# Kernel optimization log

Measured on AMD Instinct MI355X. Metric: run time of the kernel, lower is better.

The kernel has to match this reference:

```python
import jax, jax.numpy as jnp
import numpy as np

NUM_JOINTS = 17

def _build_norm_adj():
    # Same skeleton as _get_skeleton_edges, made bidirectional; row-normalized
    # so that A @ x computes the per-node mean over neighbors (every joint
    # has degree >= 1, matching the original's mean aggregation branch).
    conns = [(0, 7), (7, 8), (8, 9), (9, 10), (0, 1), (1, 2), (2, 3), (0, 4),
             (4, 5), (5, 6), (8, 11), (11, 12), (12, 13), (8, 14), (14, 15), (15, 16)]
    A = np.zeros((NUM_JOINTS, NUM_JOINTS), dtype=np.float32)
    for a, b in conns:
        A[a, b] = 1.0
        A[b, a] = 1.0
    deg = A.sum(axis=1, keepdims=True)
    A = A / np.maximum(deg, 1.0)
    return jnp.asarray(A)

def _xavier(key, out_dim, in_dim):
    lim = np.sqrt(6.0 / (in_dim + out_dim)).astype(np.float32)
    return jax.random.uniform(key, (out_dim, in_dim), jnp.float32, -lim, lim)

def setup_inputs() -> dict:
    key = jax.random.key(0)
    ks = jax.random.split(key, 6)
    B, J, D_IN, H, D_OUT = 65536, NUM_JOINTS, 3, 64, 256
    x = jax.random.normal(ks[0], (B, J, D_IN), jnp.float32)
    return {
        "x": x,
        "A": _build_norm_adj(),
        "W1": _xavier(ks[1], H, D_IN), "b1": jnp.zeros((H,), jnp.float32),
        "W2": _xavier(ks[2], H, H),    "b2": jnp.zeros((H,), jnp.float32),
        "W3": _xavier(ks[3], H, H),    "b3": jnp.zeros((H,), jnp.float32),
        "Wp1": _xavier(ks[4], H, J * H), "bp1": jnp.zeros((H,), jnp.float32),
        "Wp2": _xavier(ks[5], D_OUT, H), "bp2": jnp.zeros((D_OUT,), jnp.float32),
    }

def reference(x, A, W1, b1, W2, b2, W3, b3, Wp1, bp1, Wp2, bp2):
    # GCN layer 1: neighbor-mean aggregate then linear (+ReLU; dropout = eval identity)
    h = jnp.einsum('ij,bjd->bid', A, x)            # (B, 17, 3)
    h = jax.nn.relu(h @ W1.T + b1)                 # (B, 17, 64)
    # GCN layer 2
    h = jnp.einsum('ij,bjd->bid', A, h)
    h = jax.nn.relu(h @ W2.T + b2)
    # GCN layer 3 (no activation)
    h = jnp.einsum('ij,bjd->bid', A, h)
    h = h @ W3.T + b3                              # (B, 17, 64)
    # Global pool MLP over flattened joints
    flat = h.reshape(h.shape[0], -1)               # (B, 17*64)
    z = jax.nn.relu(flat @ Wp1.T + bp1)            # (B, 64)
    return z @ Wp2.T + bp2                         # (B, 256)
```

## Files before the change

### kernel.cpp

```cpp
#include <hip/hip_runtime.h>
#include <hip/hip_bf16.h>
#include <stdint.h>

typedef __attribute__((ext_vector_type(8))) short short8;
typedef __attribute__((ext_vector_type(4))) float f32x4;
typedef __attribute__((ext_vector_type(4))) unsigned int u32x4;
typedef __attribute__((ext_vector_type(2))) unsigned int u32x2;

constexpr int kNBR[17][4] = {
    {7, 1, 4, 0}, {0, 2, 0, 0}, {1, 3, 0, 0}, {2, 0, 0, 0},
    {0, 5, 0, 0}, {4, 6, 0, 0}, {5, 0, 0, 0}, {0, 8, 0, 0},
    {7, 9, 11, 14}, {8, 10, 0, 0}, {9, 0, 0, 0}, {8, 12, 0, 0},
    {11, 13, 0, 0}, {12, 0, 0, 0}, {8, 15, 0, 0}, {14, 16, 0, 0},
    {15, 0, 0, 0}};
constexpr int kDEG[17] = {3,2,2,1,2,2,1,2,4,2,1,2,2,1,2,2,1};
constexpr float kRDEG[5] = {0.f, 1.f, 0.5f, 0.33333334f, 0.25f};
constexpr int kWNT[4] = {3, 4, 5, 5};
constexpr int kWJT[4][5] = {{8, 1, 2, 0, 0},
                            {0, 4, 5, 3, 0},
                            {7, 9, 11, 6, 10},
                            {12, 14, 15, 13, 16}};

__device__ inline unsigned short f2bf(float f) {
  union { float f; uint32_t u; } v; v.f = f;
  uint32_t u = v.u;
  uint32_t r = u + 0x7fffu + ((u >> 16) & 1u);
  return (unsigned short)(r >> 16);
}
__device__ inline uint32_t pk2(float a, float b) {
  union { __hip_bfloat162 h; uint32_t u; } v;
  v.h = __float22bfloat162_rn(make_float2(a, b));
  return v.u;
}
__device__ inline f32x4 mfma16(short8 a, short8 b, f32x4 c) {
  return __builtin_amdgcn_mfma_f32_16x16x32_bf16(a, b, c, 0, 0, 0);
}
__device__ inline int hswz(int row, int cb) {
  return row * 128 + (cb ^ ((row & 7) << 4));
}

__global__ void prep(const float* __restrict__ W1,
                     const float* __restrict__ W2,
                     const float* __restrict__ Wp2,
                     const float* __restrict__ W3,
                     const float* __restrict__ Wp1,
                     const float* __restrict__ b3,
                     const float* __restrict__ bp1,
                     const float* __restrict__ b1,
                     short* __restrict__ W1b,
                     short* __restrict__ W2b,
                     short* __restrict__ Wp2b,
                     short* __restrict__ Mb,
                     float* __restrict__ bp1p) {
  __shared__ float w3s[4096];
  __shared__ float Qs[256];
  const int tid = threadIdx.x;
  const int bx = blockIdx.x;
  if (bx < 272) {
    for (int q = tid; q < 4096; q += 256) w3s[q] = W3[q];
    {
      int ro = tid >> 6, k = tid & 63;
      int r = bx * 4 + ro;
      int f = r / 17, i = r - f * 17;
      int dj = kDEG[i];
      float s = 0.f;
#pragma unroll
      for (int t = 0; t < 4; t++) {
        if (t < dj) {
          int nb = kNBR[i][t];
          s += kRDEG[kDEG[nb]] * Wp1[f * 1088 + nb * 64 + k];
        }
      }
      Qs[ro * 64 + k] = s;
    }
    __syncthreads();
    {
      int ro = tid >> 6, c = tid & 63;
      int r = bx * 4 + ro;
      int f = r / 17, i = r - f * 17;
      float s = 0.f;
#pragma unroll
      for (int k = 0; k < 64; k++) s += Qs[ro * 64 + k] * w3s[k * 64 + c];
      int h = c >> 5;
      int c5 = c & 31;
      int q = (c5 >> 2) & 3;
      int m = ((c5 >> 4) << 2) | (c5 & 3);
      int w = f >> 4, l15 = f & 15;
      Mb[((((w * 17 + i) * 2 + h) * 64) + q * 16 + l15) * 8 + m] = (short)f2bf(s);
    }
  } else if (bx < 354) {
    int q = (bx - 272) * 256 + tid;
    if (q < 4096) W2b[q] = (short)f2bf(W2[q]);
    int q2 = q - 4096;
    if (q2 >= 0 && q2 < 16384) Wp2b[q2] = (short)f2bf(Wp2[q2]);
    int q3 = q - 20480;
    if (q3 >= 0 && q3 < 512) {
      int k = q3 & 7, row = q3 >> 3;
      short v = 0;
      if (k < 3) v = (short)f2bf(W1[row * 3 + k]);
      else if (k == 3) v = (short)f2bf(b1[row]);
      W1b[q3] = v;
    }
  } else {
    int wv = tid >> 6, l = tid & 63;
    int f = (bx - 354) * 4 + wv;
    float s = 0.f;
#pragma unroll
    for (int i = 0; i < 17; i++) s += Wp1[f * 1088 + i * 64 + l] * b3[l];
#pragma unroll
    for (int off = 32; off > 0; off >>= 1) s += __shfl_down(s, off);
    if (l == 0) bp1p[f] = bp1[f] + s;
  }
}

template <int WV>
__device__ __forceinline__ void waveBody(
    const short* __restrict__ Mb2, const short* __restrict__ Wp2b,
    const short* __restrict__ W2b, const float* __restrict__ bp2g,
    float* __restrict__ OUT, short* hbuf, float* xs, float* sbias,
    const short8 (&w1f)[4], int bx, int lane, int ln15, int quad) {
  constexpr int NT = kWNT[WV];
  char* hb0 = (char*)hbuf;

#pragma unroll
  for (int t = 0; t < NT; t++) {
    const int j = kWJT[WV][t];
    const int dj = kDEG[j];
    const float w = kRDEG[dj];
    union { short8 s; u32x4 u; } fr[2];
#pragma unroll
    for (int g = 0; g < 2; g++) {
      const float* xsg = xs + g * 816;
      fr[g].u = (u32x4){0u, 0u, 0u, 0u};
      if (quad == 0) {
        float s0, s1, s2;
        {
          int b = ln15 * 51 + kNBR[j][0] * 3;
          s0 = xsg[b]; s1 = xsg[b + 1]; s2 = xsg[b + 2];
        }
        if (dj > 1) {
          int b = ln15 * 51 + kNBR[j][1] * 3;
          s0 += xsg[b]; s1 += xsg[b + 1]; s2 += xsg[b + 2];
        }
        if (dj > 2) {
          int b = ln15 * 51 + kNBR[j][2] * 3;
          s0 += xsg[b]; s1 += xsg[b + 1]; s2 += xsg[b + 2];
        }
        if (dj > 3) {
          int b = ln15 * 51 + kNBR[j][3] * 3;
          s0 += xsg[b]; s1 += xsg[b + 1]; s2 += xsg[b + 2];
        }
        fr[g].u.x = pk2(s0 * w, s1 * w);
        fr[g].u.y = pk2(s2 * w, 1.0f);
      }
    }
#pragma unroll
    for (int g = 0; g < 2; g++) {
      f32x4 a[4];
#pragma unroll
      for (int ft = 0; ft < 4; ft++)
        a[ft] = mfma16(w1f[ft], fr[g].s, (f32x4){0.f, 0.f, 0.f, 0.f});
#pragma unroll
      for (int ft = 0; ft < 4; ft++) {
        int fb = ft * 16 + quad * 4;
        u32x2 pk;
        pk.x = pk2(fmaxf(a[ft].x, 0.f), fmaxf(a[ft].y, 0.f));
        pk.y = pk2(fmaxf(a[ft].z, 0.f), fmaxf(a[ft].w, 0.f));
        *(u32x2*)(hb0 + g * 34816 + hswz(j * 16 + ln15, fb * 2)) = pk;
      }
    }
  }
  __syncthreads();

  short8 w2f[2][4];
#pragma unroll
  for (int kk = 0; kk < 2; kk++)
#pragma unroll
    for (int ft = 0; ft < 4; ft++)
      w2f[kk][ft] = *(const short8*)(W2b + (ft * 16 + ln15) * 64 + kk * 32 + quad * 8);

  u32x2 pkh2[2][NT][4];
#pragma unroll
  for (int t = 0; t < NT; t++) {
    const int j = kWJT[WV][t];
    const int dj = kDEG[j];
    const float w = kRDEG[dj];
#pragma unroll
    for (int g = 0; g < 2; g++) {
      f32x4 a[4];
#pragma unroll
      for (int ft = 0; ft < 4; ft++) a[ft] = (f32x4){0.f, 0.f, 0.f, 0.f};
#pragma unroll
      for (int s = 0; s < 4; s++)
        if (s < dj) {
          const int i = kNBR[j][s];
#pragma unroll
          for (int kk = 0; kk < 2; kk++) {
            short8 bf = *(const short8*)(hb0 + g * 34816 +
                                         hswz(i * 16 + ln15, kk * 64 + quad * 16));
#pragma unroll
            for (int ft = 0; ft < 4; ft++)
              a[ft] = mfma16(w2f[kk][ft], bf, a[ft]);
          }
        }
#pragma unroll
      for (int ft = 0; ft < 4; ft++) {
        int fb = ft * 16 + quad * 4;
        f32x4 bv = *(const f32x4*)&sbias[fb];
        u32x2 pk;
        pk.x = pk2(fmaxf(a[ft].x * w + bv.x, 0.f), fmaxf(a[ft].y * w + bv.y, 0.f));
        pk.y = pk2(fmaxf(a[ft].z * w + bv.z, 0.f), fmaxf(a[ft].w * w + bv.w, 0.f));
        pkh2[g][t][ft] = pk;
      }
    }
  }

  f32x4 zacc[4][2];
#pragma unroll
  for (int w4 = 0; w4 < 4; w4++) {
    zacc[w4][0] = (f32x4){0.f, 0.f, 0.f, 0.f};
    zacc[w4][1] = (f32x4){0.f, 0.f, 0.f, 0.f};
  }
  const short8* mb = (const short8*)Mb2;
#pragma unroll
  for (int t = 0; t < NT; t++) {
    const int i = kWJT[WV][t];
#pragma unroll
    for (int h = 0; h < 2; h++) {
      union { short8 s; u32x4 u; } bf0, bf1;
      bf0.u = (u32x4){pkh2[0][t][2 * h].x, pkh2[0][t][2 * h].y,
                      pkh2[0][t][2 * h + 1].x, pkh2[0][t][2 * h + 1].y};
      bf1.u = (u32x4){pkh2[1][t][2 * h].x, pkh2[1][t][2 * h].y,
                      pkh2[1][t][2 * h + 1].x, pkh2[1][t][2 * h + 1].y};
#pragma unroll
      for (int w4 = 0; w4 < 4; w4++) {
        short8 af = mb[(((w4 * 17 + i) * 2 + h) * 64) + lane];
        zacc[w4][0] = mfma16(af, bf0.s, zacc[w4][0]);
        zacc[w4][1] = mfma16(af, bf1.s, zacc[w4][1]);
      }
    }
  }
  __syncthreads();

#pragma unroll
  for (int w4 = 0; w4 < 4; w4++)
#pragma unroll
    for (int g = 0; g < 2; g++)
      *(f32x4*)(hb0 + WV * 8192 + (w4 * 2 + g) * 1024 + lane * 16) = zacc[w4][g];

  short8 wp2f[4][2];
#pragma unroll
  for (int t = 0; t < 4; t++) {
    int ot = WV + 4 * t;
    wp2f[t][0] = *(const short8*)(Wp2b + (ot * 16 + ln15) * 64 + quad * 8);
    wp2f[t][1] = *(const short8*)(Wp2b + (ot * 16 + ln15) * 64 + 32 + quad * 8);
  }
  __syncthreads();

  char* zbB = (char*)xs;
#pragma unroll
  for (int half = 0; half < 2; half++) {
    const int gw = WV + half * 4;
    const int g = gw & 1, w4 = gw >> 1;
    f32x4 s0 = *(const f32x4*)(hb0 + 0 * 8192 + gw * 1024 + lane * 16);
    f32x4 s1 = *(const f32x4*)(hb0 + 1 * 8192 + gw * 1024 + lane * 16);
    f32x4 s2 = *(const f32x4*)(hb0 + 2 * 8192 + gw * 1024 + lane * 16);
    f32x4 s3 = *(const f32x4*)(hb0 + 3 * 8192 + gw * 1024 + lane * 16);
    f32x4 s = (s0 + s1) + (s2 + s3);
    const int e = lane & 15, qd = lane >> 4;
    const int f0 = w4 * 16 + qd * 4;
    f32x4 bv = *(const f32x4*)&sbias[64 + f0];
    u32x2 pk;
    pk.x = pk2(fmaxf(s.x + bv.x, 0.f), fmaxf(s.y + bv.y, 0.f));
    pk.y = pk2(fmaxf(s.z + bv.z, 0.f), fmaxf(s.w + bv.w, 0.f));
    *(u32x2*)(zbB + g * 2048 + e * 128 + ((f0 * 2) ^ ((e & 7) << 4))) = pk;
  }
  __syncthreads();

  const int e0 = bx * 32;
#pragma unroll
  for (int g = 0; g < 2; g++) {
    short8 bf0 = *(const short8*)(zbB + g * 2048 + ln15 * 128 +
                                  ((quad * 16) ^ ((ln15 & 7) << 4)));
    short8 bf1 = *(const short8*)(zbB + g * 2048 + ln15 * 128 +
                                  ((64 + quad * 16) ^ ((ln15 & 7) << 4)));
    int e0g = e0 + g * 16;
#pragma unroll
    for (int t = 0; t < 4; t++) {
      int ot = WV + 4 * t;
      f32x4 a = mfma16(wp2f[t][0], bf0, (f32x4){0.f, 0.f, 0.f, 0.f});
      a = mfma16(wp2f[t][1], bf1, a);
      int ob = ot * 16 + quad * 4;
      f32x4 bv = *(const f32x4*)&bp2g[ob];
      f32x4 res = a + bv;
      *(f32x4*)(OUT + (size_t)(e0g + ln15) * 256 + ob) = res;
    }
  }
}

__launch_bounds__(256, 2)
__global__ void gcn_main(const float* __restrict__ X,
                         const short* __restrict__ Mb2,
                         const short* __restrict__ Wp2b,
                         const short* __restrict__ W2b,
                         const short* __restrict__ W1b,
                         const float* __restrict__ bp1p,
                         const float* __restrict__ b2g,
                         const float* __restrict__ bp2g,
                         float* __restrict__ OUT) {
  __shared__ __align__(16) short hbuf[2 * 272 * 64];
  __shared__ __align__(16) float xs[2 * 816];
  __shared__ __align__(16) float sbias[128];

  const int tid = threadIdx.x;
  const int wave = tid >> 6;
  const int lane = tid & 63;
  const int ln15 = lane & 15;
  const int quad = lane >> 4;
  const int bx = blockIdx.x;

  for (int q = tid; q < 408; q += 256)
    ((f32x4*)xs)[q] = ((const f32x4*)(X + (size_t)bx * 1632))[q];
  short8 w1f[4];
#pragma unroll
  for (int ft = 0; ft < 4; ft++)
    w1f[ft] = *(const short8*)(W1b + (ft * 16 + ln15) * 8);
  if (tid < 128) sbias[tid] = (tid < 64) ? b2g[tid] : bp1p[tid - 64];
  __syncthreads();

  if (wave == 0)
    waveBody<0>(Mb2, Wp2b, W2b, bp2g, OUT, hbuf, xs, sbias, w1f, bx, lane, ln15, quad);
  else if (wave == 1)
    waveBody<1>(Mb2, Wp2b, W2b, bp2g, OUT, hbuf, xs, sbias, w1f, bx, lane, ln15, quad);
  else if (wave == 2)
    waveBody<2>(Mb2, Wp2b, W2b, bp2g, OUT, hbuf, xs, sbias, w1f, bx, lane, ln15, quad);
  else
    waveBody<3>(Mb2, Wp2b, W2b, bp2g, OUT, hbuf, xs, sbias, w1f, bx, lane, ln15, quad);
}

extern "C" void kernel_launch(void* const* d_in, const int* in_sizes, int n_in,
                              void* d_out, int out_size, void* d_ws, size_t ws_size,
                              hipStream_t stream) {
  const float* X = (const float*)d_in[0];
  const float* W1 = (const float*)d_in[2];
  const float* b1 = (const float*)d_in[3];
  const float* W2 = (const float*)d_in[4];
  const float* b2 = (const float*)d_in[5];
  const float* W3 = (const float*)d_in[6];
  const float* b3 = (const float*)d_in[7];
  const float* Wp1 = (const float*)d_in[8];
  const float* bp1 = (const float*)d_in[9];
  const float* Wp2 = (const float*)d_in[10];
  const float* bp2 = (const float*)d_in[11];
  float* OUT = (float*)d_out;
  const int B = in_sizes[0] / 51;

  char* ws = (char*)d_ws;
  short* Mb = (short*)(ws + 0);
  short* Wp2b = (short*)(ws + 139264);
  short* W2b = (short*)(ws + 172032);
  short* W1b = (short*)(ws + 180224);
  float* bp1p = (float*)(ws + 181248);

  prep<<<370, 256, 0, stream>>>(W1, W2, Wp2, W3, Wp1, b3, bp1, b1,
                                W1b, W2b, Wp2b, Mb, bp1p);
  gcn_main<<<B / 32, 256, 0, stream>>>(X, Mb, Wp2b, W2b, W1b, bp1p,
                                       b2, bp2, OUT);
}
```

Baseline: 148.6 us.

## Recompute layer-1 activations per wave in registers instead of sharing through LDS

Each wave now recomputes the layer-1 GCN outputs for every neighbor of its assigned joints directly in registers, so layer-2 MFMAs read them without a shared-memory round trip. This drops the 70KB hbuf and two block-wide barriers. The final pooled-MLP bias/ReLU stage also keeps its result in registers, with W2 and Wp2 permuted in prep so the MFMA output fragment can be reused directly as the next B operand. In exchange, layer-1 MFMAs are duplicated per neighbor and register pressure rises from the ph1 arrays.

```diff
diff --git a/kernel.cpp b/kernel.cpp
--- a/kernel.cpp
+++ b/kernel.cpp
@@ -34,9 +34,6 @@
 }
 __device__ inline f32x4 mfma16(short8 a, short8 b, f32x4 c) {
   return __builtin_amdgcn_mfma_f32_16x16x32_bf16(a, b, c, 0, 0, 0);
-}
-__device__ inline int hswz(int row, int cb) {
-  return row * 128 + (cb ^ ((row & 7) << 4));
 }
 
 __global__ void prep(const float* __restrict__ W1,
@@ -90,9 +87,19 @@
     }
   } else if (bx < 354) {
     int q = (bx - 272) * 256 + tid;
-    if (q < 4096) W2b[q] = (short)f2bf(W2[q]);
+    if (q < 4096) {
+      int r = q >> 6, c = q & 63;
+      int h = c >> 5, c5 = c & 31;
+      int qq = (c5 >> 2) & 3, m = ((c5 >> 4) << 2) | (c5 & 3);
+      W2b[r * 64 + h * 32 + qq * 8 + m] = (short)f2bf(W2[q]);
+    }
     int q2 = q - 4096;
-    if (q2 >= 0 && q2 < 16384) Wp2b[q2] = (short)f2bf(Wp2[q2]);
+    if (q2 >= 0 && q2 < 16384) {
+      int r = q2 >> 6, c = q2 & 63;
+      int h = c >> 5, c5 = c & 31;
+      int qq = (c5 >> 2) & 3, m = ((c5 >> 4) << 2) | (c5 & 3);
+      Wp2b[r * 64 + h * 32 + qq * 8 + m] = (short)f2bf(Wp2[q2]);
+    }
     int q3 = q - 20480;
     if (q3 >= 0 && q3 < 512) {
       int k = q3 & 7, row = q3 >> 3;
@@ -115,92 +122,89 @@
 
 template <int WV>
 __device__ __forceinline__ void waveBody(
-    const short* __restrict__ Mb2, const short* __restrict__ Wp2b,
-    const short* __restrict__ W2b, const float* __restrict__ bp2g,
-    float* __restrict__ OUT, short* hbuf, float* xs, float* sbias,
+    const short* __restrict__ Mb2, const short* __restrict__ Wp2p,
+    const short* __restrict__ W2p, const float* __restrict__ bp2g,
+    float* __restrict__ OUT, float* __restrict__ pbuf,
+    float* __restrict__ xs, float* __restrict__ sbias,
     const short8 (&w1f)[4], int bx, int lane, int ln15, int quad) {
   constexpr int NT = kWNT[WV];
-  char* hb0 = (char*)hbuf;
-
+
+  short8 w2f[2][4];
+#pragma unroll
+  for (int h = 0; h < 2; h++)
+#pragma unroll
+    for (int ft = 0; ft < 4; ft++)
+      w2f[h][ft] = *(const short8*)(W2p + (ft * 16 + ln15) * 64 + h * 32 + quad * 8);
+
+  u32x2 pkh2[2][NT][4];
 #pragma unroll
   for (int t = 0; t < NT; t++) {
     const int j = kWJT[WV][t];
     const int dj = kDEG[j];
-    const float w = kRDEG[dj];
-    union { short8 s; u32x4 u; } fr[2];
-#pragma unroll
-    for (int g = 0; g < 2; g++) {
-      const float* xsg = xs + g * 816;
-      fr[g].u = (u32x4){0u, 0u, 0u, 0u};
-      if (quad == 0) {
-        float s0, s1, s2;
-        {
-          int b = ln15 * 51 + kNBR[j][0] * 3;
-          s0 = xsg[b]; s1 = xsg[b + 1]; s2 = xsg[b + 2];
+    const float wj = kRDEG[dj];
+    u32x2 ph1[4][2][4];
+#pragma unroll
+    for (int s = 0; s < 4; s++) {
+      if (s < dj) {
+        const int i = kNBR[j][s];
+        const int di = kDEG[i];
+        const float wi = kRDEG[di];
+#pragma unroll
+        for (int g = 0; g < 2; g++) {
+          const float* xsg = xs + g * 816;
+          union { short8 s8; u32x4 u; } fr;
+          fr.u = (u32x4){0u, 0u, 0u, 0u};
+          if (quad == 0) {
+            float s0, s1, s2;
+            {
+              int b = ln15 * 51 + kNBR[i][0] * 3;
+              s0 = xsg[b]; s1 = xsg[b + 1]; s2 = xsg[b + 2];
+            }
+            if (di > 1) {
+              int b = ln15 * 51 + kNBR[i][1] * 3;
+              s0 += xsg[b]; s1 += xsg[b + 1]; s2 += xsg[b + 2];
+            }
+            if (di > 2) {
+              int b = ln15 * 51 + kNBR[i][2] * 3;
+              s0 += xsg[b]; s1 += xsg[b + 1]; s2 += xsg[b + 2];
+            }
+            if (di > 3) {
+              int b = ln15 * 51 + kNBR[i][3] * 3;
+              s0 += xsg[b]; s1 += xsg[b + 1]; s2 += xsg[b + 2];
+            }
+            fr.u.x = pk2(s0 * wi, s1 * wi);
+            fr.u.y = pk2(s2 * wi, 1.0f);
+          }
+          f32x4 a[4];
+#pragma unroll
+          for (int ft = 0; ft < 4; ft++)
+            a[ft] = mfma16(w1f[ft], fr.s8, (f32x4){0.f, 0.f, 0.f, 0.f});
+#pragma unroll
+          for (int ft = 0; ft < 4; ft++) {
+            u32x2 pk;
+            pk.x = pk2(fmaxf(a[ft].x, 0.f), fmaxf(a[ft].y, 0.f));
+            pk.y = pk2(fmaxf(a[ft].z, 0.f), fmaxf(a[ft].w, 0.f));
+            ph1[s][g][ft] = pk;
+          }
         }
-        if (dj > 1) {
-          int b = ln15 * 51 + kNBR[j][1] * 3;
-          s0 += xsg[b]; s1 += xsg[b + 1]; s2 += xsg[b + 2];
-        }
-        if (dj > 2) {
-          int b = ln15 * 51 + kNBR[j][2] * 3;
-          s0 += xsg[b]; s1 += xsg[b + 1]; s2 += xsg[b + 2];
-        }
-        if (dj > 3) {
-          int b = ln15 * 51 + kNBR[j][3] * 3;
-          s0 += xsg[b]; s1 += xsg[b + 1]; s2 += xsg[b + 2];
-        }
-        fr[g].u.x = pk2(s0 * w, s1 * w);
-        fr[g].u.y = pk2(s2 * w, 1.0f);
       }
     }
 #pragma unroll
     for (int g = 0; g < 2; g++) {
       f32x4 a[4];
 #pragma unroll
-      for (int ft = 0; ft < 4; ft++)
-        a[ft] = mfma16(w1f[ft], fr[g].s, (f32x4){0.f, 0.f, 0.f, 0.f});
-#pragma unroll
-      for (int ft = 0; ft < 4; ft++) {
-        int fb = ft * 16 + quad * 4;
-        u32x2 pk;
-        pk.x = pk2(fmaxf(a[ft].x, 0.f), fmaxf(a[ft].y, 0.f));
-        pk.y = pk2(fmaxf(a[ft].z, 0.f), fmaxf(a[ft].w, 0.f));
-        *(u32x2*)(hb0 + g * 34816 + hswz(j * 16 + ln15, fb * 2)) = pk;
-      }
-    }
-  }
-  __syncthreads();
-
-  short8 w2f[2][4];
-#pragma unroll
-  for (int kk = 0; kk < 2; kk++)
-#pragma unroll
-    for (int ft = 0; ft < 4; ft++)
-      w2f[kk][ft] = *(const short8*)(W2b + (ft * 16 + ln15) * 64 + kk * 32 + quad * 8);
-
-  u32x2 pkh2[2][NT][4];
-#pragma unroll
-  for (int t = 0; t < NT; t++) {
-    const int j = kWJT[WV][t];
-    const int dj = kDEG[j];
-    const float w = kRDEG[dj];
-#pragma unroll
-    for (int g = 0; g < 2; g++) {
-      f32x4 a[4];
-#pragma unroll
       for (int ft = 0; ft < 4; ft++) a[ft] = (f32x4){0.f, 0.f, 0.f, 0.f};
 #pragma unroll
       for (int s = 0; s < 4; s++)
         if (s < dj) {
-          const int i = kNBR[j][s];
-#pragma unroll
-          for (int kk = 0; kk < 2; kk++) {
-            short8 bf = *(const short8*)(hb0 + g * 34816 +
-                                         hswz(i * 16 + ln15, kk * 64 + quad * 16));
+#pragma unroll
+          for (int h = 0; h < 2; h++) {
+            union { short8 s8; u32x4 u; } bf;
+            bf.u = (u32x4){ph1[s][g][2 * h].x, ph1[s][g][2 * h].y,
+                           ph1[s][g][2 * h + 1].x, ph1[s][g][2 * h + 1].y};
 #pragma unroll
             for (int ft = 0; ft < 4; ft++)
-              a[ft] = mfma16(w2f[kk][ft], bf, a[ft]);
+              a[ft] = mfma16(w2f[h][ft], bf.s8, a[ft]);
           }
         }
 #pragma unroll
@@ -208,8 +212,8 @@
         int fb = ft * 16 + quad * 4;
         f32x4 bv = *(const f32x4*)&sbias[fb];
         u32x2 pk;
-        pk.x = pk2(fmaxf(a[ft].x * w + bv.x, 0.f), fmaxf(a[ft].y * w + bv.y, 0.f));
-        pk.y = pk2(fmaxf(a[ft].z * w + bv.z, 0.f), fmaxf(a[ft].w * w + bv.w, 0.f));
+        pk.x = pk2(fmaxf(a[ft].x * wj + bv.x, 0.f), fmaxf(a[ft].y * wj + bv.y, 0.f));
+        pk.y = pk2(fmaxf(a[ft].z * wj + bv.z, 0.f), fmaxf(a[ft].w * wj + bv.w, 0.f));
         pkh2[g][t][ft] = pk;
       }
     }
@@ -227,7 +231,7 @@
     const int i = kWJT[WV][t];
 #pragma unroll
     for (int h = 0; h < 2; h++) {
-      union { short8 s; u32x4 u; } bf0, bf1;
+      union { short8 s8; u32x4 u; } bf0, bf1;
       bf0.u = (u32x4){pkh2[0][t][2 * h].x, pkh2[0][t][2 * h].y,
                       pkh2[0][t][2 * h + 1].x, pkh2[0][t][2 * h + 1].y};
       bf1.u = (u32x4){pkh2[1][t][2 * h].x, pkh2[1][t][2 * h].y,
@@ -235,61 +239,56 @@
 #pragma unroll
       for (int w4 = 0; w4 < 4; w4++) {
         short8 af = mb[(((w4 * 17 + i) * 2 + h) * 64) + lane];
-        zacc[w4][0] = mfma16(af, bf0.s, zacc[w4][0]);
-        zacc[w4][1] = mfma16(af, bf1.s, zacc[w4][1]);
+        zacc[w4][0] = mfma16(af, bf0.s8, zacc[w4][0]);
+        zacc[w4][1] = mfma16(af, bf1.s8, zacc[w4][1]);
       }
     }
   }
-  __syncthreads();
-
 #pragma unroll
   for (int w4 = 0; w4 < 4; w4++)
 #pragma unroll
     for (int g = 0; g < 2; g++)
-      *(f32x4*)(hb0 + WV * 8192 + (w4 * 2 + g) * 1024 + lane * 16) = zacc[w4][g];
-
+      *(f32x4*)(pbuf + WV * 2048 + (w4 * 2 + g) * 256 + lane * 4) = zacc[w4][g];
   short8 wp2f[4][2];
 #pragma unroll
   for (int t = 0; t < 4; t++) {
     int ot = WV + 4 * t;
-    wp2f[t][0] = *(const short8*)(Wp2b + (ot * 16 + ln15) * 64 + quad * 8);
-    wp2f[t][1] = *(const short8*)(Wp2b + (ot * 16 + ln15) * 64 + 32 + quad * 8);
+    wp2f[t][0] = *(const short8*)(Wp2p + (ot * 16 + ln15) * 64 + quad * 8);
+    wp2f[t][1] = *(const short8*)(Wp2p + (ot * 16 + ln15) * 64 + 32 + quad * 8);
   }
   __syncthreads();
 
-  char* zbB = (char*)xs;
-#pragma unroll
-  for (int half = 0; half < 2; half++) {
-    const int gw = WV + half * 4;
-    const int g = gw & 1, w4 = gw >> 1;
-    f32x4 s0 = *(const f32x4*)(hb0 + 0 * 8192 + gw * 1024 + lane * 16);
-    f32x4 s1 = *(const f32x4*)(hb0 + 1 * 8192 + gw * 1024 + lane * 16);
-    f32x4 s2 = *(const f32x4*)(hb0 + 2 * 8192 + gw * 1024 + lane * 16);
-    f32x4 s3 = *(const f32x4*)(hb0 + 3 * 8192 + gw * 1024 + lane * 16);
-    f32x4 s = (s0 + s1) + (s2 + s3);
-    const int e = lane & 15, qd = lane >> 4;
-    const int f0 = w4 * 16 + qd * 4;
-    f32x4 bv = *(const f32x4*)&sbias[64 + f0];
-    u32x2 pk;
-    pk.x = pk2(fmaxf(s.x + bv.x, 0.f), fmaxf(s.y + bv.y, 0.f));
-    pk.y = pk2(fmaxf(s.z + bv.z, 0.f), fmaxf(s.w + bv.w, 0.f));
-    *(u32x2*)(zbB + g * 2048 + e * 128 + ((f0 * 2) ^ ((e & 7) << 4))) = pk;
-  }
-  __syncthreads();
+  u32x2 zp[2][4];
+#pragma unroll
+  for (int w4 = 0; w4 < 4; w4++) {
+    f32x4 bv = *(const f32x4*)&sbias[64 + w4 * 16 + quad * 4];
+#pragma unroll
+    for (int g = 0; g < 2; g++) {
+      const int gw = w4 * 2 + g;
+      f32x4 s0 = *(const f32x4*)(pbuf + 0 * 2048 + gw * 256 + lane * 4);
+      f32x4 s1 = *(const f32x4*)(pbuf + 1 * 2048 + gw * 256 + lane * 4);
+      f32x4 s2 = *(const f32x4*)(pbuf + 2 * 2048 + gw * 256 + lane * 4);
+      f32x4 s3 = *(const f32x4*)(pbuf + 3 * 2048 + gw * 256 + lane * 4);
+      f32x4 s = (s0 + s1) + (s2 + s3);
+      u32x2 pk;
+      pk.x = pk2(fmaxf(s.x + bv.x, 0.f), fmaxf(s.y + bv.y, 0.f));
+      pk.y = pk2(fmaxf(s.z + bv.z, 0.f), fmaxf(s.w + bv.w, 0.f));
+      zp[g][w4] = pk;
+    }
+  }
 
   const int e0 = bx * 32;
 #pragma unroll
   for (int g = 0; g < 2; g++) {
-    short8 bf0 = *(const short8*)(zbB + g * 2048 + ln15 * 128 +
-                                  ((quad * 16) ^ ((ln15 & 7) << 4)));
-    short8 bf1 = *(const short8*)(zbB + g * 2048 + ln15 * 128 +
-                                  ((64 + quad * 16) ^ ((ln15 & 7) << 4)));
+    union { short8 s8; u32x4 u; } bf0, bf1;
+    bf0.u = (u32x4){zp[g][0].x, zp[g][0].y, zp[g][1].x, zp[g][1].y};
+    bf1.u = (u32x4){zp[g][2].x, zp[g][2].y, zp[g][3].x, zp[g][3].y};
     int e0g = e0 + g * 16;
 #pragma unroll
     for (int t = 0; t < 4; t++) {
       int ot = WV + 4 * t;
-      f32x4 a = mfma16(wp2f[t][0], bf0, (f32x4){0.f, 0.f, 0.f, 0.f});
-      a = mfma16(wp2f[t][1], bf1, a);
+      f32x4 a = mfma16(wp2f[t][0], bf0.s8, (f32x4){0.f, 0.f, 0.f, 0.f});
+      a = mfma16(wp2f[t][1], bf1.s8, a);
       int ob = ot * 16 + quad * 4;
       f32x4 bv = *(const f32x4*)&bp2g[ob];
       f32x4 res = a + bv;
@@ -301,14 +300,14 @@
 __launch_bounds__(256, 2)
 __global__ void gcn_main(const float* __restrict__ X,
                          const short* __restrict__ Mb2,
-                         const short* __restrict__ Wp2b,
-                         const short* __restrict__ W2b,
+                         const short* __restrict__ Wp2p,
+                         const short* __restrict__ W2p,
                          const short* __restrict__ W1b,
                          const float* __restrict__ bp1p,
                          const float* __restrict__ b2g,
                          const float* __restrict__ bp2g,
                          float* __restrict__ OUT) {
-  __shared__ __align__(16) short hbuf[2 * 272 * 64];
+  __shared__ __align__(16) float pbuf[8192];
   __shared__ __align__(16) float xs[2 * 816];
   __shared__ __align__(16) float sbias[128];
 
@@ -329,13 +328,13 @@
   __syncthreads();
 
   if (wave == 0)
-    waveBody<0>(Mb2, Wp2b, W2b, bp2g, OUT, hbuf, xs, sbias, w1f, bx, lane, ln15, quad);
+    waveBody<0>(Mb2, Wp2p, W2p, bp2g, OUT, pbuf, xs, sbias, w1f, bx, lane, ln15, quad);
   else if (wave == 1)
-    waveBody<1>(Mb2, Wp2b, W2b, bp2g, OUT, hbuf, xs, sbias, w1f, bx, lane, ln15, quad);
+    waveBody<1>(Mb2, Wp2p, W2p, bp2g, OUT, pbuf, xs, sbias, w1f, bx, lane, ln15, quad);
   else if (wave == 2)
-    waveBody<2>(Mb2, Wp2b, W2b, bp2g, OUT, hbuf, xs, sbias, w1f, bx, lane, ln15, quad);
+    waveBody<2>(Mb2, Wp2p, W2p, bp2g, OUT, pbuf, xs, sbias, w1f, bx, lane, ln15, quad);
   else
-    waveBody<3>(Mb2, Wp2b, W2b, bp2g, OUT, hbuf, xs, sbias, w1f, bx, lane, ln15, quad);
+    waveBody<3>(Mb2, Wp2p, W2p, bp2g, OUT, pbuf, xs, sbias, w1f, bx, lane, ln15, quad);
 }
 
 extern "C" void kernel_launch(void* const* d_in, const int* in_sizes, int n_in,
```

New measurement: 147.6 us. Within noise of the previous version (-0.7%).
